# Optimization experiments

Measured on AMD Instinct MI355X. Metric: run time of the kernel, lower is better.

## Reference

```python
import jax, jax.numpy as jnp
import numpy as np

N, E = 100000, 600000
IN, H = 164, 128
NH = 4  # attention heads over embed_dim H//4 = 32


def layer_norm(x, g, b, eps=1e-5):
    m = x.mean(-1, keepdims=True)
    v = x.var(-1, keepdims=True)
    return (x - m) * jax.lax.rsqrt(v + eps) * g + b


def gcn_conv(x, W, b, src, dst, n):
    # PyG GCNConv: add self-loops, symmetric D^{-1/2}(A+I)D^{-1/2} normalization.
    deg = jnp.ones((n,), x.dtype).at[dst].add(1.0)  # degree of A+I on target nodes
    dinv = jax.lax.rsqrt(deg)
    xw = x @ W  # [n, out]
    msg = xw[src] * (dinv[src] * dinv[dst])[:, None]  # gather + edge-norm
    agg = jax.ops.segment_sum(msg, dst, num_segments=n)  # scatter-add
    agg = agg + xw * (dinv * dinv)[:, None]  # self-loop term
    return agg + b


def mha_seq1(x, Wq, bq, Wk, bk, Wv, bv, Wo, bo):
    # nn.MultiheadAttention with seq_len==1: softmax over a single key -> weights==1.
    dh = x.shape[-1] // NH
    q = (x @ Wq + bq).reshape(-1, NH, dh)
    k = (x @ Wk + bk).reshape(-1, NH, dh)
    v = (x @ Wv + bv).reshape(-1, NH, dh)
    scores = jnp.sum(q * k, -1, keepdims=True) / jnp.sqrt(jnp.float32(dh))  # [n,NH,1]
    attn = jax.nn.softmax(scores[..., None], axis=-1)[..., 0]  # all ones, kept for fidelity
    out = (attn * v).reshape(-1, NH * dh)
    return out @ Wo + bo


def setup_inputs() -> dict:
    key = jax.random.key(0)
    ks = jax.random.split(key, 16)

    def kaiming(k, i, o):
        return jax.random.normal(k, (i, o), jnp.float32) * (2.0 / i) ** 0.5

    Ha, Hb, Hc = H, H // 2, H // 4  # 128, 64, 32
    return {
        "x": jax.random.normal(ks[0], (N, IN), jnp.float32),
        "edge_index": jax.random.randint(ks[1], (2, E), 0, N),
        "Wi": kaiming(ks[2], IN, Ha), "bi": jnp.zeros((Ha,), jnp.float32),
        "g1": jnp.ones((Ha,), jnp.float32), "b1": jnp.zeros((Ha,), jnp.float32),
        "Wg1": kaiming(ks[3], Ha, Ha), "bg1": jnp.zeros((Ha,), jnp.float32),
        "Wg2": kaiming(ks[4], Ha, Hb), "bg2": jnp.zeros((Hb,), jnp.float32),
        "g2": jnp.ones((Hb,), jnp.float32), "b2": jnp.zeros((Hb,), jnp.float32),
        "Wg3": kaiming(ks[5], Hb, Hc), "bg3": jnp.zeros((Hc,), jnp.float32),
        "Wq": kaiming(ks[6], Hc, Hc), "bq": jnp.zeros((Hc,), jnp.float32),
        "Wk": kaiming(ks[7], Hc, Hc), "bk": jnp.zeros((Hc,), jnp.float32),
        "Wv": kaiming(ks[8], Hc, Hc), "bv": jnp.zeros((Hc,), jnp.float32),
        "Wo": kaiming(ks[9], Hc, Hc), "bo": jnp.zeros((Hc,), jnp.float32),
        "Wc1": kaiming(ks[10], Hc, H // 8), "bc1": jnp.zeros((H // 8,), jnp.float32),
        "Wc2": kaiming(ks[11], H // 8, 32), "bc2": jnp.zeros((32,), jnp.float32),
        "Wc3": kaiming(ks[12], 32, 1), "bc3": jnp.zeros((1,), jnp.float32),
    }


def reference(x, edge_index, Wi, bi, g1, b1, Wg1, bg1, Wg2, bg2, g2, b2,
              Wg3, bg3, Wq, bq, Wk, bk, Wv, bv, Wo, bo,
              Wc1, bc1, Wc2, bc2, Wc3, bc3):
    src, dst = edge_index[0], edge_index[1]
    n = x.shape[0]
    # dropout layers are identity in eval mode
    h = layer_norm(jax.nn.relu(x @ Wi + bi), g1, b1)
    h1 = jax.nn.relu(gcn_conv(h, Wg1, bg1, src, dst, n)) + h
    h2 = layer_norm(jax.nn.relu(gcn_conv(h1, Wg2, bg2, src, dst, n)), g2, b2)
    h3 = jax.nn.relu(gcn_conv(h2, Wg3, bg3, src, dst, n))
    h3 = mha_seq1(h3, Wq, bq, Wk, bk, Wv, bv, Wo, bo)
    h3 = jax.nn.relu(h3 @ Wc1 + bc1)
    h3 = jax.nn.relu(h3 @ Wc2 + bc2)
    return (h3 @ Wc3 + bc3)[:, 0]
```

## Files before the change

### kernel.cpp

```cpp
#include <hip/hip_runtime.h>


typedef __attribute__((ext_vector_type(8))) _Float16 f16x8;
typedef __attribute__((ext_vector_type(4))) _Float16 f16x4;
typedef __attribute__((ext_vector_type(4))) float f32x4;

__global__ void k_count(const int* __restrict__ dst, int* __restrict__ counts, int e) {
  int i = blockIdx.x * blockDim.x + threadIdx.x;
  if (i < e) atomicAdd(&counts[dst[i]], 1);
}

__global__ __launch_bounds__(256) void k_scan_part(
    const int* __restrict__ counts, int* __restrict__ bsums, int n) {
  int tid = threadIdx.x;
  int i0 = blockIdx.x * 1024 + tid * 4;
  int s = 0;
#pragma unroll
  for (int k = 0; k < 4; k++) { int i = i0 + k; if (i < n) s += counts[i]; }
#pragma unroll
  for (int d = 1; d < 64; d <<= 1) s += __shfl_xor(s, d);
  __shared__ int wsum[4];
  int lane = tid & 63, w = tid >> 6;
  if (lane == 0) wsum[w] = s;
  __syncthreads();
  if (tid == 0) bsums[blockIdx.x] = wsum[0] + wsum[1] + wsum[2] + wsum[3];
}

__global__ __launch_bounds__(128) void k_scan_top(int* __restrict__ bsums, int nb) {
  int tid = threadIdx.x;
  int orig = (tid < nb) ? bsums[tid] : 0;
  int v = orig;
  int lane = tid & 63, w = tid >> 6;
#pragma unroll
  for (int d = 1; d < 64; d <<= 1) { int t = __shfl_up(v, d); if (lane >= d) v += t; }
  __shared__ int ws[2];
  if (lane == 63) ws[w] = v;
  __syncthreads();
  if (w == 1) v += ws[0];
  if (tid < nb) bsums[tid] = v - orig;
}

__global__ __launch_bounds__(256) void k_scan_down(
    int* __restrict__ counts, const int* __restrict__ bsums,
    int* __restrict__ offsets, float* __restrict__ dinv, int n, int e) {
  int tid = threadIdx.x;
  int i0 = blockIdx.x * 1024 + tid * 4;
  int c[4]; int tsum = 0;
#pragma unroll
  for (int k = 0; k < 4; k++) { int i = i0 + k; c[k] = (i < n) ? counts[i] : 0; tsum += c[k]; }
  int v = tsum;
  int lane = tid & 63, w = tid >> 6;
#pragma unroll
  for (int d = 1; d < 64; d <<= 1) { int t = __shfl_up(v, d); if (lane >= d) v += t; }
  __shared__ int wsum[4];
  if (lane == 63) wsum[w] = v;
  __syncthreads();
  int wadd = 0;
#pragma unroll
  for (int q = 0; q < 4; q++) if (q < w) wadd += wsum[q];
  int run = (v - tsum) + wadd + bsums[blockIdx.x];
#pragma unroll
  for (int k = 0; k < 4; k++) {
    int i = i0 + k;
    if (i < n) {
      offsets[i] = run;
      dinv[i] = rsqrtf((float)(c[k] + 1));
      counts[i] = 0;
    }
    run += c[k];
  }
  if (blockIdx.x == 0 && tid == 0) offsets[n] = e;
}

__global__ void k_fill(const int* __restrict__ src, const int* __restrict__ dst,
                       const int* __restrict__ offsets, int* __restrict__ cursor,
                       const float* __restrict__ dinv, int2* __restrict__ csr, int e) {
  int i = blockIdx.x * blockDim.x + threadIdx.x;
  if (i >= e) return;
  int s = src[i], d = dst[i];
  int pos = atomicAdd(&cursor[d], 1);
  csr[offsets[d] + pos] = make_int2(s, __float_as_int(dinv[s] * dinv[d]));
}

__device__ __forceinline__ void pack_hi(const float* __restrict__ W,
                                        _Float16* __restrict__ dst,
                                        int K, int N, int u) {
  int lane = u & 63; int rest = u >> 6; int CT = N >> 4;
  int ct = rest % CT, ks = rest / CT;
  int gcol = ct * 16 + (lane & 15);
  int gk0 = ks * 32 + (lane >> 4) * 8;
  size_t o = (size_t)(ks * CT + ct) * 512 + lane * 8;
#pragma unroll
  for (int i = 0; i < 8; i++) {
    float v = (gk0 + i < K) ? W[(size_t)(gk0 + i) * N + gcol] : 0.0f;
    dst[o + i] = (_Float16)v;
  }
}

__global__ void k_setup(const float* __restrict__ Wi, const float* __restrict__ Wg1,
                        const float* __restrict__ Wg2, const float* __restrict__ Wg3,
                        _Float16* __restrict__ pWi, _Float16* __restrict__ pWg1,
                        _Float16* __restrict__ pWg2, _Float16* __restrict__ pWg3,
                        int* __restrict__ counts, int n) {
  int b = blockIdx.x;
  if (b < 25) {
    int t = b * 256 + threadIdx.x;
    if (t < 3072) pack_hi(Wi, pWi, 164, 128, t);
    else if (t < 5120) pack_hi(Wg1, pWg1, 128, 128, t - 3072);
    else if (t < 6144) pack_hi(Wg2, pWg2, 128, 64, t - 5120);
    else if (t < 6400) pack_hi(Wg3, pWg3, 64, 32, t - 6144);
  } else {
    int i = (b - 25) * 256 + threadIdx.x;
    if (i < n) counts[i] = 0;
  }
}

__global__ __launch_bounds__(512, 4) void k_gemm_in(
    const float* __restrict__ x, const _Float16* __restrict__ pB,
    const float* __restrict__ bias, const float* __restrict__ gamma,
    const float* __restrict__ beta, _Float16* __restrict__ out, int n) {
  constexpr int K = 164, N = 128, CT = 8;
  int tid = threadIdx.x;
  int lane = tid & 63, w = tid >> 6;
  int row = blockIdx.x * 128 + w * 16 + (lane & 15);
  bool rv = row < n;
  int kof = (lane >> 4) * 8;
  const f16x8* Bf = (const f16x8*)pB;
  f32x4 acc[CT];
#pragma unroll
  for (int c = 0; c < CT; c++) acc[c] = (f32x4)0.0f;
#pragma unroll
  for (int ks = 0; ks < 6; ks++) {
    int gk = ks * 32 + kof;
    float v[8];
    if (rv && gk + 8 <= K) {
      const float4* p = (const float4*)(x + (size_t)row * K + gk);
      float4 u0 = p[0], u1 = p[1];
      v[0] = u0.x; v[1] = u0.y; v[2] = u0.z; v[3] = u0.w;
      v[4] = u1.x; v[5] = u1.y; v[6] = u1.z; v[7] = u1.w;
    } else if (rv && gk < K) {
      float4 u0 = *(const float4*)(x + (size_t)row * K + gk);
      v[0] = u0.x; v[1] = u0.y; v[2] = u0.z; v[3] = u0.w;
      v[4] = 0.f; v[5] = 0.f; v[6] = 0.f; v[7] = 0.f;
    } else {
#pragma unroll
      for (int i = 0; i < 8; i++) v[i] = 0.0f;
    }
    f16x8 ah, al;
#pragma unroll
    for (int i = 0; i < 8; i++) {
      ah[i] = (_Float16)v[i];
      al[i] = (_Float16)(v[i] - (float)ah[i]);
    }
#pragma unroll
    for (int c = 0; c < CT; c++) {
      f16x8 b = Bf[(ks * CT + c) * 64 + lane];
      acc[c] = __builtin_amdgcn_mfma_f32_16x16x32_f16(ah, b, acc[c], 0, 0, 0);
      acc[c] = __builtin_amdgcn_mfma_f32_16x16x32_f16(al, b, acc[c], 0, 0, 0);
    }
  }
  int r0 = (lane >> 4) * 4;
  int li = lane & 15;
  float s1[4] = {0, 0, 0, 0}, s2[4] = {0, 0, 0, 0};
#pragma unroll
  for (int c = 0; c < CT; c++) {
    float bb = bias[c * 16 + li];
#pragma unroll
    for (int r = 0; r < 4; r++) {
      float t = acc[c][r] + bb;
      t = t > 0.0f ? t : 0.0f;
      acc[c][r] = t;
      s1[r] += t;
      s2[r] += t * t;
    }
  }
#pragma unroll
  for (int m = 1; m < 16; m <<= 1) {
#pragma unroll
    for (int r = 0; r < 4; r++) {
      s1[r] += __shfl_xor(s1[r], m);
      s2[r] += __shfl_xor(s2[r], m);
    }
  }
#pragma unroll
  for (int c = 0; c < CT; c++) {
    float gv = gamma[c * 16 + li], bv = beta[c * 16 + li];
#pragma unroll
    for (int r = 0; r < 4; r++) {
      int node = blockIdx.x * 128 + w * 16 + r0 + r;
      if (node < n) {
        float mean = s1[r] * (1.0f / N);
        float var = s2[r] * (1.0f / N) - mean * mean;
        float rs = rsqrtf(var + 1e-5f);
        out[(size_t)node * N + c * 16 + li] =
            (_Float16)((acc[c][r] - mean) * rs * gv + bv);
      }
    }
  }
}

template <int K, int N>
__global__ __launch_bounds__(512, 4) void k_gemm_f16(
    const _Float16* __restrict__ A, const _Float16* __restrict__ pB,
    _Float16* __restrict__ out, int n) {
  constexpr int KS = K / 32, CT = N / 16;
  int tid = threadIdx.x;
  int lane = tid & 63, w = tid >> 6;
  int row = blockIdx.x * 128 + w * 16 + (lane & 15);
  bool rv = row < n;
  const _Float16* ar = A + (size_t)row * K + (lane >> 4) * 8;
  const f16x8* Bf = (const f16x8*)pB;
  f16x8 av[KS];
#pragma unroll
  for (int ks = 0; ks < KS; ks++) {
    if (rv) av[ks] = *(const f16x8*)(ar + ks * 32);
    else {
#pragma unroll
      for (int i = 0; i < 8; i++) av[ks][i] = (_Float16)0.0f;
    }
  }
  f32x4 acc[CT];
#pragma unroll
  for (int c = 0; c < CT; c++) acc[c] = (f32x4)0.0f;
#pragma unroll
  for (int ks = 0; ks < KS; ks++) {
#pragma unroll
    for (int c = 0; c < CT; c++) {
      f16x8 b = Bf[(ks * CT + c) * 64 + lane];
      acc[c] = __builtin_amdgcn_mfma_f32_16x16x32_f16(av[ks], b, acc[c], 0, 0, 0);
    }
  }
  int r0 = (lane >> 4) * 4;
  int li = lane & 15;
#pragma unroll
  for (int c = 0; c < CT; c++) {
#pragma unroll
    for (int r = 0; r < 4; r++) {
      int node = blockIdx.x * 128 + w * 16 + r0 + r;
      if (node < n) out[(size_t)node * N + c * 16 + li] = (_Float16)acc[c][r];
    }
  }
}

template <int OUT_D, int MODE>
__global__ __launch_bounds__(256, 2) void k_gather(
    const int* __restrict__ off, const int2* __restrict__ csr,
    const _Float16* __restrict__ xw, const float* __restrict__ dinv,
    const float* __restrict__ bias, const _Float16* __restrict__ auxh,
    const float* __restrict__ gamma, const float* __restrict__ beta,
    _Float16* __restrict__ out, int n) {
  constexpr int TPN = OUT_D / 4;
  constexpr int NPB = 256 / TPN;
  int tid = threadIdx.x;
  int node = blockIdx.x * NPB + tid / TPN;
  int li = tid % TPN;
  if (node >= n) return;
  int start = off[node], end = off[node + 1];
  float di = dinv[node];
  float d2 = di * di;
  const _Float16* xp = xw + 4 * li;
  f16x4 self = *(const f16x4*)(xp + (size_t)node * OUT_D);
  f16x4 hres;
  if constexpr (MODE == 0)
    hres = *(const f16x4*)(auxh + (size_t)node * OUT_D + 4 * li);
  float a0 = (float)self[0] * d2 + bias[4 * li + 0];
  float a1 = (float)self[1] * d2 + bias[4 * li + 1];
  float a2 = (float)self[2] * d2 + bias[4 * li + 2];
  float a3 = (float)self[3] * d2 + bias[4 * li + 3];
  for (int cb = start; cb < end; cb += TPN) {
    int m = end - cb; if (m > TPN) m = TPN;
    int sv = node; float nv = 0.0f;
    if (li < m) { int2 me = csr[cb + li]; sv = me.x; nv = __int_as_float(me.y); }
    for (int j0 = 0; j0 < m; j0 += 8) {
      int s0 = __shfl(sv, j0 + 0, TPN), s1 = __shfl(sv, j0 + 1, TPN);
      int s2 = __shfl(sv, j0 + 2, TPN), s3 = __shfl(sv, j0 + 3, TPN);
      int s4 = __shfl(sv, j0 + 4, TPN), s5 = __shfl(sv, j0 + 5, TPN);
      int s6 = __shfl(sv, j0 + 6, TPN), s7 = __shfl(sv, j0 + 7, TPN);
      float w0 = __shfl(nv, j0 + 0, TPN), w1 = __shfl(nv, j0 + 1, TPN);
      float w2 = __shfl(nv, j0 + 2, TPN), w3 = __shfl(nv, j0 + 3, TPN);
      float w4 = __shfl(nv, j0 + 4, TPN), w5 = __shfl(nv, j0 + 5, TPN);
      float w6 = __shfl(nv, j0 + 6, TPN), w7 = __shfl(nv, j0 + 7, TPN);
      f16x4 v0 = *(const f16x4*)(xp + (size_t)s0 * OUT_D);
      f16x4 v1 = *(const f16x4*)(xp + (size_t)s1 * OUT_D);
      f16x4 v2 = *(const f16x4*)(xp + (size_t)s2 * OUT_D);
      f16x4 v3 = *(const f16x4*)(xp + (size_t)s3 * OUT_D);
      f16x4 v4 = *(const f16x4*)(xp + (size_t)s4 * OUT_D);
      f16x4 v5 = *(const f16x4*)(xp + (size_t)s5 * OUT_D);
      f16x4 v6 = *(const f16x4*)(xp + (size_t)s6 * OUT_D);
      f16x4 v7 = *(const f16x4*)(xp + (size_t)s7 * OUT_D);
      a0 += (float)v0[0] * w0 + (float)v1[0] * w1 + (float)v2[0] * w2 + (float)v3[0] * w3
          + (float)v4[0] * w4 + (float)v5[0] * w5 + (float)v6[0] * w6 + (float)v7[0] * w7;
      a1 += (float)v0[1] * w0 + (float)v1[1] * w1 + (float)v2[1] * w2 + (float)v3[1] * w3
          + (float)v4[1] * w4 + (float)v5[1] * w5 + (float)v6[1] * w6 + (float)v7[1] * w7;
      a2 += (float)v0[2] * w0 + (float)v1[2] * w1 + (float)v2[2] * w2 + (float)v3[2] * w3
          + (float)v4[2] * w4 + (float)v5[2] * w5 + (float)v6[2] * w6 + (float)v7[2] * w7;
      a3 += (float)v0[3] * w0 + (float)v1[3] * w1 + (float)v2[3] * w2 + (float)v3[3] * w3
          + (float)v4[3] * w4 + (float)v5[3] * w5 + (float)v6[3] * w6 + (float)v7[3] * w7;
    }
  }
  _Float16* po = out + (size_t)node * OUT_D + 4 * li;
  if constexpr (MODE == 0) {
    f16x4 o;
    o[0] = (_Float16)((a0 > 0.0f ? a0 : 0.0f) + (float)hres[0]);
    o[1] = (_Float16)((a1 > 0.0f ? a1 : 0.0f) + (float)hres[1]);
    o[2] = (_Float16)((a2 > 0.0f ? a2 : 0.0f) + (float)hres[2]);
    o[3] = (_Float16)((a3 > 0.0f ? a3 : 0.0f) + (float)hres[3]);
    *(f16x4*)po = o;
  } else if constexpr (MODE == 1) {
    float v0 = a0 > 0.0f ? a0 : 0.0f, v1 = a1 > 0.0f ? a1 : 0.0f;
    float v2 = a2 > 0.0f ? a2 : 0.0f, v3 = a3 > 0.0f ? a3 : 0.0f;
    float s1 = v0 + v1 + v2 + v3;
    float s2 = v0 * v0 + v1 * v1 + v2 * v2 + v3 * v3;
#pragma unroll
    for (int d = 1; d < TPN; d <<= 1) {
      s1 += __shfl_xor(s1, d, TPN);
      s2 += __shfl_xor(s2, d, TPN);
    }
    float m_ = s1 * (1.0f / OUT_D);
    float var = s2 * (1.0f / OUT_D) - m_ * m_;
    float rs = rsqrtf(var + 1e-5f);
    f16x4 o;
    o[0] = (_Float16)((v0 - m_) * rs * gamma[4 * li + 0] + beta[4 * li + 0]);
    o[1] = (_Float16)((v1 - m_) * rs * gamma[4 * li + 1] + beta[4 * li + 1]);
    o[2] = (_Float16)((v2 - m_) * rs * gamma[4 * li + 2] + beta[4 * li + 2]);
    o[3] = (_Float16)((v3 - m_) * rs * gamma[4 * li + 3] + beta[4 * li + 3]);
    *(f16x4*)po = o;
  } else {
    f16x4 o;
    o[0] = (_Float16)a0; o[1] = (_Float16)a1;
    o[2] = (_Float16)a2; o[3] = (_Float16)a3;
    *(f16x4*)po = o;
  }
}

__global__ __launch_bounds__(256) void k_tail(
    const _Float16* __restrict__ agg3, const float* __restrict__ Wv,
    const float* __restrict__ bv, const float* __restrict__ Wo,
    const float* __restrict__ bo, const float* __restrict__ Wc1,
    const float* __restrict__ bc1, const float* __restrict__ Wc2,
    const float* __restrict__ bc2, const float* __restrict__ Wc3,
    const float* __restrict__ bc3, float* __restrict__ out, int n) {
  __shared__ float sWv[1024], sWo[1024], sWc1[512], sWc2[512];
  __shared__ float sbv[32], sbo[32], sbc2[32], sWc3[32], sbc1[16], sbc3[1];
  int tid = threadIdx.x;
  for (int i = tid; i < 1024; i += 256) { sWv[i] = Wv[i]; sWo[i] = Wo[i]; }
  for (int i = tid; i < 512; i += 256) { sWc1[i] = Wc1[i]; sWc2[i] = Wc2[i]; }
  if (tid < 32) { sbv[tid] = bv[tid]; sbo[tid] = bo[tid];
                  sbc2[tid] = bc2[tid]; sWc3[tid] = Wc3[tid]; }
  if (tid < 16) sbc1[tid] = bc1[tid];
  if (tid == 0) sbc3[0] = bc3[0];
  __syncthreads();
  int node = blockIdx.x * blockDim.x + tid;
  if (node >= n) return;
  float a[32];
  const f16x8* row8 = (const f16x8*)(agg3 + (size_t)node * 32);
#pragma unroll
  for (int q = 0; q < 4; q++) {
    f16x8 t = row8[q];
#pragma unroll
    for (int i = 0; i < 8; i++) {
      float f = (float)t[i];
      a[8 * q + i] = f > 0.0f ? f : 0.0f;
    }
  }
  float v[32];
#pragma unroll
  for (int j = 0; j < 32; j++) v[j] = sbv[j];
  for (int k = 0; k < 32; k++) {
#pragma unroll
    for (int j = 0; j < 32; j++) v[j] += a[k] * sWv[k * 32 + j];
  }
  float o[32];
#pragma unroll
  for (int j = 0; j < 32; j++) o[j] = sbo[j];
  for (int k = 0; k < 32; k++) {
#pragma unroll
    for (int j = 0; j < 32; j++) o[j] += v[k] * sWo[k * 32 + j];
  }
  float c1[16];
#pragma unroll
  for (int j = 0; j < 16; j++) c1[j] = sbc1[j];
  for (int k = 0; k < 32; k++) {
#pragma unroll
    for (int j = 0; j < 16; j++) c1[j] += o[k] * sWc1[k * 16 + j];
  }
#pragma unroll
  for (int j = 0; j < 16; j++) c1[j] = c1[j] > 0.0f ? c1[j] : 0.0f;
  float c2[32];
#pragma unroll
  for (int j = 0; j < 32; j++) c2[j] = sbc2[j];
  for (int k = 0; k < 16; k++) {
#pragma unroll
    for (int j = 0; j < 32; j++) c2[j] += c1[k] * sWc2[k * 32 + j];
  }
  float r = sbc3[0];
#pragma unroll
  for (int k = 0; k < 32; k++) {
    float c = c2[k] > 0.0f ? c2[k] : 0.0f;
    r += c * sWc3[k];
  }
  out[node] = r;
}

extern "C" void kernel_launch(void* const* d_in, const int* in_sizes, int n_in,
                              void* d_out, int out_size, void* d_ws, size_t ws_size,
                              hipStream_t stream) {
  const float* x   = (const float*)d_in[0];
  const int* ei    = (const int*)d_in[1];
  const float* Wi  = (const float*)d_in[2];
  const float* bi  = (const float*)d_in[3];
  const float* g1  = (const float*)d_in[4];
  const float* b1  = (const float*)d_in[5];
  const float* Wg1 = (const float*)d_in[6];
  const float* bg1 = (const float*)d_in[7];
  const float* Wg2 = (const float*)d_in[8];
  const float* bg2 = (const float*)d_in[9];
  const float* g2  = (const float*)d_in[10];
  const float* b2  = (const float*)d_in[11];
  const float* Wg3 = (const float*)d_in[12];
  const float* bg3 = (const float*)d_in[13];
  const float* Wv  = (const float*)d_in[18];
  const float* bv  = (const float*)d_in[19];
  const float* Wo  = (const float*)d_in[20];
  const float* bo  = (const float*)d_in[21];
  const float* Wc1 = (const float*)d_in[22];
  const float* bc1 = (const float*)d_in[23];
  const float* Wc2 = (const float*)d_in[24];
  const float* bc2 = (const float*)d_in[25];
  const float* Wc3 = (const float*)d_in[26];
  const float* bc3 = (const float*)d_in[27];

  const int n = in_sizes[0] / 164;
  const int e = in_sizes[1] / 2;
  const int* src = ei;
  const int* dst = ei + e;

  char* ws = (char*)d_ws;
  size_t off = 0;
  auto alloc = [&](size_t bytes) {
    char* p = ws + off;
    off += (bytes + 255) & ~(size_t)255;
    return p;
  };
  _Float16* A     = (_Float16*)alloc((size_t)n * 128 * 2);
  _Float16* B     = (_Float16*)alloc((size_t)n * 128 * 2);
  _Float16* C     = (_Float16*)alloc((size_t)n * 128 * 2);
  float* dinv     = (float*)alloc((size_t)n * 4);
  int*   counts   = (int*)alloc((size_t)n * 4);
  int*   offsets  = (int*)alloc((size_t)(n + 1) * 4);
  int*   bsums    = (int*)alloc(128 * 4);
  int2*  csr      = (int2*)alloc((size_t)e * 8);
  _Float16* pWi   = (_Float16*)alloc(3072 * 16);
  _Float16* pWg1  = (_Float16*)alloc(2048 * 16);
  _Float16* pWg2  = (_Float16*)alloc(1024 * 16);
  _Float16* pWg3  = (_Float16*)alloc(256 * 16);
  (void)ws_size;

  const int BS = 256;
  const int SB = (n + 1023) / 1024;
  const int GB = (n + 127) / 128;

  k_setup<<<25 + (n + 255) / 256, 256, 0, stream>>>(
      Wi, Wg1, Wg2, Wg3, pWi, pWg1, pWg2, pWg3, counts, n);

  k_count<<<(e + BS - 1) / BS, BS, 0, stream>>>(dst, counts, e);
  k_scan_part<<<SB, 256, 0, stream>>>(counts, bsums, n);
  k_scan_top<<<1, 128, 0, stream>>>(bsums, SB);
  k_scan_down<<<SB, 256, 0, stream>>>(counts, bsums, offsets, dinv, n, e);
  k_fill<<<(e + BS - 1) / BS, BS, 0, stream>>>(src, dst, offsets, counts, dinv,
                                               csr, e);

  k_gemm_in<<<GB, 512, 0, stream>>>(x, pWi, bi, g1, b1, A, n);

  k_gemm_f16<128, 128><<<GB, 512, 0, stream>>>(A, pWg1, B, n);
  k_gather<128, 0><<<(n + 7) / 8, 256, 0, stream>>>(
      offsets, csr, B, dinv, bg1, A, nullptr, nullptr, C, n);

  k_gemm_f16<128, 64><<<GB, 512, 0, stream>>>(C, pWg2, A, n);
  k_gather<64, 1><<<(n + 15) / 16, 256, 0, stream>>>(
      offsets, csr, A, dinv, bg2, nullptr, g2, b2, B, n);

  k_gemm_f16<64, 32><<<GB, 512, 0, stream>>>(B, pWg3, A, n);
  k_gather<32, 2><<<(n + 31) / 32, 256, 0, stream>>>(
      offsets, csr, A, dinv, bg3, nullptr, nullptr, nullptr, C, n);

  k_tail<<<(n + BS - 1) / BS, BS, 0, stream>>>(
      C, Wv, bv, Wo, bo, Wc1, bc1, Wc2, bc2, Wc3, bc3, (float*)d_out, n);
}
```

Measured before the change: 234.3 us.

## Stage GEMM A-tiles through LDS with async global_load_lds double buffering

The input and feature-transform GEMM kernels now load their A operand through LDS using global_load_lds with a double buffer. The next K-slice is prefetched while the current one feeds MFMA, and a zero pad buffer stands in for out-of-range rows and the ragged K tail. The aim is coalesced, asynchronous row loads that overlap with compute, replacing per-lane strided register loads. The cost is two barriers per K-step, added LDS use that may limit occupancy, and reliance on hand-written vmcnt waits being correct.

```diff
diff --git a/kernel.cpp b/kernel.cpp
--- a/kernel.cpp
+++ b/kernel.cpp
@@ -4,6 +4,21 @@
 typedef __attribute__((ext_vector_type(8))) _Float16 f16x8;
 typedef __attribute__((ext_vector_type(4))) _Float16 f16x4;
 typedef __attribute__((ext_vector_type(4))) float f32x4;
+
+#define GLOAD_LDS16(gp, lp)                                        \
+  __builtin_amdgcn_global_load_lds(                                \
+      (const __attribute__((address_space(1))) void*)(gp),         \
+      (__attribute__((address_space(3))) void*)(lp), 16, 0, 0)
+
+static __device__ __forceinline__ void wait_vm0() {
+  asm volatile("s_waitcnt vmcnt(0)" ::: "memory");
+}
+static __device__ __forceinline__ void wait_vm1() {
+  asm volatile("s_waitcnt vmcnt(1)" ::: "memory");
+}
+static __device__ __forceinline__ void wait_vm2() {
+  asm volatile("s_waitcnt vmcnt(2)" ::: "memory");
+}
 
 __global__ void k_count(const int* __restrict__ dst, int* __restrict__ counts, int e) {
   int i = blockIdx.x * blockDim.x + threadIdx.x;
@@ -101,7 +116,7 @@
                         const float* __restrict__ Wg2, const float* __restrict__ Wg3,
                         _Float16* __restrict__ pWi, _Float16* __restrict__ pWg1,
                         _Float16* __restrict__ pWg2, _Float16* __restrict__ pWg3,
-                        int* __restrict__ counts, int n) {
+                        int* __restrict__ counts, float* __restrict__ zp, int n) {
   int b = blockIdx.x;
   if (b < 25) {
     int t = b * 256 + threadIdx.x;
@@ -110,6 +125,7 @@
     else if (t < 6144) pack_hi(Wg2, pWg2, 128, 64, t - 5120);
     else if (t < 6400) pack_hi(Wg3, pWg3, 64, 32, t - 6144);
   } else {
+    if (b == 25 && threadIdx.x < 64) zp[threadIdx.x] = 0.0f;
     int i = (b - 25) * 256 + threadIdx.x;
     if (i < n) counts[i] = 0;
   }
@@ -118,34 +134,43 @@
 __global__ __launch_bounds__(512, 4) void k_gemm_in(
     const float* __restrict__ x, const _Float16* __restrict__ pB,
     const float* __restrict__ bias, const float* __restrict__ gamma,
-    const float* __restrict__ beta, _Float16* __restrict__ out, int n) {
-  constexpr int K = 164, N = 128, CT = 8;
+    const float* __restrict__ beta, const float* __restrict__ zp,
+    _Float16* __restrict__ out, int n) {
+  constexpr int N = 128, CT = 8;
+  __shared__ __align__(16) float sA[2][128 * 32];
   int tid = threadIdx.x;
   int lane = tid & 63, w = tid >> 6;
-  int row = blockIdx.x * 128 + w * 16 + (lane & 15);
-  bool rv = row < n;
-  int kof = (lane >> 4) * 8;
+  int base = blockIdx.x * 128;
   const f16x8* Bf = (const f16x8*)pB;
+
+  auto stage = [&](int ks, int buf) {
+#pragma unroll
+    for (int j = 0; j < 2; j++) {
+      int q = (j * 8 + w) * 64 + lane;
+      int row = q >> 3;
+      int c = q & 7;
+      int rg = base + row;
+      const void* src = (rg < n && (ks < 5 || c == 0))
+                            ? (const void*)(x + (size_t)rg * 164 + ks * 32 + c * 4)
+                            : (const void*)zp;
+      GLOAD_LDS16(src, &sA[buf][(size_t)(j * 8 + w) * 256]);
+    }
+  };
+
   f32x4 acc[CT];
 #pragma unroll
   for (int c = 0; c < CT; c++) acc[c] = (f32x4)0.0f;
+
+  stage(0, 0);
 #pragma unroll
   for (int ks = 0; ks < 6; ks++) {
-    int gk = ks * 32 + kof;
-    float v[8];
-    if (rv && gk + 8 <= K) {
-      const float4* p = (const float4*)(x + (size_t)row * K + gk);
-      float4 u0 = p[0], u1 = p[1];
-      v[0] = u0.x; v[1] = u0.y; v[2] = u0.z; v[3] = u0.w;
-      v[4] = u1.x; v[5] = u1.y; v[6] = u1.z; v[7] = u1.w;
-    } else if (rv && gk < K) {
-      float4 u0 = *(const float4*)(x + (size_t)row * K + gk);
-      v[0] = u0.x; v[1] = u0.y; v[2] = u0.z; v[3] = u0.w;
-      v[4] = 0.f; v[5] = 0.f; v[6] = 0.f; v[7] = 0.f;
-    } else {
-#pragma unroll
-      for (int i = 0; i < 8; i++) v[i] = 0.0f;
-    }
+    if (ks + 1 < 6) { stage(ks + 1, (ks + 1) & 1); wait_vm2(); }
+    else wait_vm0();
+    __builtin_amdgcn_s_barrier();
+    const float4* fr = (const float4*)&sA[ks & 1][((w * 16 + (lane & 15)) * 32) +
+                                                 (lane >> 4) * 8];
+    float4 u0 = fr[0], u1 = fr[1];
+    float v[8] = {u0.x, u0.y, u0.z, u0.w, u1.x, u1.y, u1.z, u1.w};
     f16x8 ah, al;
 #pragma unroll
     for (int i = 0; i < 8; i++) {
@@ -158,7 +183,9 @@
       acc[c] = __builtin_amdgcn_mfma_f32_16x16x32_f16(ah, b, acc[c], 0, 0, 0);
       acc[c] = __builtin_amdgcn_mfma_f32_16x16x32_f16(al, b, acc[c], 0, 0, 0);
     }
-  }
+    __builtin_amdgcn_s_barrier();
+  }
+
   int r0 = (lane >> 4) * 4;
   int li = lane & 15;
   float s1[4] = {0, 0, 0, 0}, s2[4] = {0, 0, 0, 0};
@@ -187,7 +214,7 @@
     float gv = gamma[c * 16 + li], bv = beta[c * 16 + li];
 #pragma unroll
     for (int r = 0; r < 4; r++) {
-      int node = blockIdx.x * 128 + w * 16 + r0 + r;
+      int node = base + w * 16 + r0 + r;
       if (node < n) {
         float mean = s1[r] * (1.0f / N);
         float var = s2[r] * (1.0f / N) - mean * mean;
@@ -202,41 +229,51 @@
 template <int K, int N>
 __global__ __launch_bounds__(512, 4) void k_gemm_f16(
     const _Float16* __restrict__ A, const _Float16* __restrict__ pB,
-    _Float16* __restrict__ out, int n) {
+    const float* __restrict__ zp, _Float16* __restrict__ out, int n) {
   constexpr int KS = K / 32, CT = N / 16;
+  __shared__ __align__(16) _Float16 sA[2][128 * 32];
   int tid = threadIdx.x;
   int lane = tid & 63, w = tid >> 6;
-  int row = blockIdx.x * 128 + w * 16 + (lane & 15);
-  bool rv = row < n;
-  const _Float16* ar = A + (size_t)row * K + (lane >> 4) * 8;
+  int base = blockIdx.x * 128;
   const f16x8* Bf = (const f16x8*)pB;
-  f16x8 av[KS];
+
+  auto stage = [&](int ks, int buf) {
+    int q = w * 64 + lane;
+    int row = q >> 2;
+    int c = q & 3;
+    int rg = base + row;
+    const void* src = (rg < n) ? (const void*)(A + (size_t)rg * K + ks * 32 + c * 8)
+                               : (const void*)zp;
+    GLOAD_LDS16(src, &sA[buf][(size_t)w * 512]);
+  };
+
+  f32x4 acc[CT];
+#pragma unroll
+  for (int c = 0; c < CT; c++) acc[c] = (f32x4)0.0f;
+
+  stage(0, 0);
 #pragma unroll
   for (int ks = 0; ks < KS; ks++) {
-    if (rv) av[ks] = *(const f16x8*)(ar + ks * 32);
-    else {
-#pragma unroll
-      for (int i = 0; i < 8; i++) av[ks][i] = (_Float16)0.0f;
-    }
-  }
-  f32x4 acc[CT];
-#pragma unroll
-  for (int c = 0; c < CT; c++) acc[c] = (f32x4)0.0f;
-#pragma unroll
-  for (int ks = 0; ks < KS; ks++) {
+    if (ks + 1 < KS) { stage(ks + 1, (ks + 1) & 1); wait_vm1(); }
+    else wait_vm0();
+    __builtin_amdgcn_s_barrier();
+    f16x8 av = *(const f16x8*)&sA[ks & 1][((w * 16 + (lane & 15)) * 32) +
+                                          (lane >> 4) * 8];
 #pragma unroll
     for (int c = 0; c < CT; c++) {
       f16x8 b = Bf[(ks * CT + c) * 64 + lane];
-      acc[c] = __builtin_amdgcn_mfma_f32_16x16x32_f16(av[ks], b, acc[c], 0, 0, 0);
-    }
-  }
+      acc[c] = __builtin_amdgcn_mfma_f32_16x16x32_f16(av, b, acc[c], 0, 0, 0);
+    }
+    __builtin_amdgcn_s_barrier();
+  }
+
   int r0 = (lane >> 4) * 4;
   int li = lane & 15;
 #pragma unroll
   for (int c = 0; c < CT; c++) {
 #pragma unroll
     for (int r = 0; r < 4; r++) {
-      int node = blockIdx.x * 128 + w * 16 + r0 + r;
+      int node = base + w * 16 + r0 + r;
       if (node < n) out[(size_t)node * N + c * 16 + li] = (_Float16)acc[c][r];
     }
   }
@@ -454,6 +491,7 @@
   _Float16* pWg1  = (_Float16*)alloc(2048 * 16);
   _Float16* pWg2  = (_Float16*)alloc(1024 * 16);
   _Float16* pWg3  = (_Float16*)alloc(256 * 16);
+  float* zp       = (float*)alloc(64 * 4);
   (void)ws_size;
 
   const int BS = 256;
@@ -461,7 +499,7 @@
   const int GB = (n + 127) / 128;
 
   k_setup<<<25 + (n + 255) / 256, 256, 0, stream>>>(
-      Wi, Wg1, Wg2, Wg3, pWi, pWg1, pWg2, pWg3, counts, n);
+      Wi, Wg1, Wg2, Wg3, pWi, pWg1, pWg2, pWg3, counts, zp, n);
 
   k_count<<<(e + BS - 1) / BS, BS, 0, stream>>>(dst, counts, e);
   k_scan_part<<<SB, 256, 0, stream>>>(counts, bsums, n);
@@ -470,17 +508,17 @@
   k_fill<<<(e + BS - 1) / BS, BS, 0, stream>>>(src, dst, offsets, counts, dinv,
                                                csr, e);
 
-  k_gemm_in<<<GB, 512, 0, stream>>>(x, pWi, bi, g1, b1, A, n);
-
-  k_gemm_f16<128, 128><<<GB, 512, 0, stream>>>(A, pWg1, B, n);
+  k_gemm_in<<<GB, 512, 0, stream>>>(x, pWi, bi, g1, b1, zp, A, n);
+
+  k_gemm_f16<128, 128><<<GB, 512, 0, stream>>>(A, pWg1, zp, B, n);
   k_gather<128, 0><<<(n + 7) / 8, 256, 0, stream>>>(
       offsets, csr, B, dinv, bg1, A, nullptr, nullptr, C, n);
 
-  k_gemm_f16<128, 64><<<GB, 512, 0, stream>>>(C, pWg2, A, n);
+  k_gemm_f16<128, 64><<<GB, 512, 0, stream>>>(C, pWg2, zp, A, n);
   k_gather<64, 1><<<(n + 15) / 16, 256, 0, stream>>>(
       offsets, csr, A, dinv, bg2, nullptr, g2, b2, B, n);
 
-  k_gemm_f16<64, 32><<<GB, 512, 0, stream>>>(B, pWg3, A, n);
+  k_gemm_f16<64, 32><<<GB, 512, 0, stream>>>(B, pWg3, zp, A, n);
   k_gather<32, 2><<<(n + 31) / 32, 256, 0, stream>>>(
       offsets, csr, A, dinv, bg3, nullptr, nullptr, nullptr, C, n);
 
```

After: 237.0 us. Within noise of the previous version (+1.2%).
